# Performance work log

Measured on AMD Instinct MI355X. Metric: run time of the kernel, lower is better.

Reference implementation:

```python
import jax, jax.numpy as jnp
import numpy as np

VOCAB, H, HEADS, S, FF = 100, 8, 2, 6, 16
HD = H // HEADS  # head_dim = 4
EPS = 1e-5


def _layernorm(x, g, b):
    mu = jnp.mean(x, axis=-1, keepdims=True)
    var = jnp.mean((x - mu) ** 2, axis=-1, keepdims=True)
    return (x - mu) * jax.lax.rsqrt(var + EPS) * g + b


def setup_inputs() -> dict:
    key = jax.random.key(0)
    ks = jax.random.split(key, 20)
    B = 262144
    d = {
        'input_ids': jax.random.randint(ks[0], (B, S), 0, VOCAB),
        'tok_emb': jax.random.normal(ks[1], (VOCAB, H), jnp.float32) * 0.02,
        'pos_emb': jax.random.normal(ks[2], (S, H), jnp.float32) * 0.02,
        'Wq': jax.random.normal(ks[3], (H, H), jnp.float32) * 0.1,
        'bq': jnp.zeros((H,), jnp.float32),
        'Wk': jax.random.normal(ks[4], (H, H), jnp.float32) * 0.1,
        'bk': jnp.zeros((H,), jnp.float32),
        'Wv': jax.random.normal(ks[5], (H, H), jnp.float32) * 0.1,
        'bv': jnp.zeros((H,), jnp.float32),
        'Wo': jax.random.normal(ks[6], (H, H), jnp.float32) * 0.1,
        'bo': jnp.zeros((H,), jnp.float32),
        'W1': jax.random.normal(ks[7], (FF, H), jnp.float32) * 0.1,
        'b1': jnp.zeros((FF,), jnp.float32),
        'W2': jax.random.normal(ks[8], (H, FF), jnp.float32) * 0.1,
        'b2': jnp.zeros((H,), jnp.float32),
        'g1': jnp.ones((H,), jnp.float32),
        'be1': jnp.zeros((H,), jnp.float32),
        'g2': jnp.ones((H,), jnp.float32),
        'be2': jnp.zeros((H,), jnp.float32),
    }
    return d


def reference(input_ids, tok_emb, pos_emb, Wq, bq, Wk, bk, Wv, bv, Wo, bo,
              W1, b1, W2, b2, g1, be1, g2, be2):
    B, Sq = input_ids.shape
    x = tok_emb[input_ids] + pos_emb[None, :, :]  # [B,S,H]
    q = x @ Wq.T + bq
    k = x @ Wk.T + bk
    v = x @ Wv.T + bv
    # split heads: [B, heads, S, head_dim]
    q = q.reshape(B, Sq, HEADS, HD).transpose(0, 2, 1, 3)
    k = k.reshape(B, Sq, HEADS, HD).transpose(0, 2, 1, 3)
    v = v.reshape(B, Sq, HEADS, HD).transpose(0, 2, 1, 3)
    scores = jnp.einsum('bhsd,bhtd->bhst', q, k) / (HD ** 0.5)
    probs = jax.nn.softmax(scores, axis=-1)
    attn = jnp.einsum('bhst,bhtd->bhsd', probs, v)
    attn = attn.transpose(0, 2, 1, 3).reshape(B, Sq, H)
    attn = attn @ Wo.T + bo
    h = _layernorm(x + attn, g1, be1)
    ffn = jax.nn.gelu(h @ W1.T + b1, approximate=False) @ W2.T + b2
    return _layernorm(h + ffn, g2, be2)
```

## Files before the change

kernel.cpp:

```cpp
#include <hip/hip_runtime.h>

#define TT_S 6
#define TT_H 8
#define TT_FF 16
#define SEQ_PER_BLK 64
#define BLK 384
#define KV_STRIDE_U 52

typedef __fp16 h2_t __attribute__((ext_vector_type(2)));
typedef __fp16 h8_t __attribute__((ext_vector_type(8)));

__device__ __forceinline__ unsigned pk2(float a, float b) {
  h2_t h = __builtin_amdgcn_cvt_pkrtz(a, b);
  return __builtin_bit_cast(unsigned, h);
}

__global__ __launch_bounds__(BLK, 6) void tt_fused(
    const int* __restrict__ ids,
    const float* __restrict__ tok_emb, const float* __restrict__ pos_emb,
    const float* __restrict__ Wq, const float* __restrict__ bq,
    const float* __restrict__ Wk, const float* __restrict__ bk,
    const float* __restrict__ Wv, const float* __restrict__ bv,
    const float* __restrict__ Wo, const float* __restrict__ bo,
    const float* __restrict__ W1, const float* __restrict__ b1,
    const float* __restrict__ W2, const float* __restrict__ b2,
    const float* __restrict__ g1, const float* __restrict__ be1,
    const float* __restrict__ g2, const float* __restrict__ be2,
    float* __restrict__ out, int B)
{
  __shared__ __align__(16) unsigned s_kv[SEQ_PER_BLK * KV_STRIDE_U];
  __shared__ __align__(16) unsigned s_tok[400];

  const int tid = threadIdx.x;
  for (int i = tid; i < 400; i += BLK) {
    float2 tv = ((const float2*)tok_emb)[i];
    s_tok[i] = pk2(tv.x, tv.y);
  }
  __syncthreads();

  const int s_loc = tid / TT_S;
  const int t     = tid - s_loc * TT_S;
  const int seq_g = blockIdx.x * SEQ_PER_BLK + s_loc;
  const bool valid = (seq_g < B);
  const size_t gidx = (size_t)blockIdx.x * BLK + tid;
  const int id = valid ? ids[gidx] : 0;

  h8_t t0 = ((const h8_t*)s_tok)[id];
  const float4* pr = (const float4*)(pos_emb + t * TT_H);
  float4 p0 = pr[0];
  float4 p1 = pr[1];
  float xs[TT_H];
  xs[0] = (float)t0[0] + p0.x; xs[1] = (float)t0[1] + p0.y;
  xs[2] = (float)t0[2] + p0.z; xs[3] = (float)t0[3] + p0.w;
  xs[4] = (float)t0[4] + p1.x; xs[5] = (float)t0[5] + p1.y;
  xs[6] = (float)t0[6] + p1.z; xs[7] = (float)t0[7] + p1.w;

  {
    float kr[TT_H], vr[TT_H];
    #pragma unroll
    for (int i = 0; i < TT_H; ++i) {
      float ak = bk[i], av = bv[i];
      #pragma unroll
      for (int j = 0; j < TT_H; ++j) {
        ak = fmaf(xs[j], Wk[i*8+j], ak);
        av = fmaf(xs[j], Wv[i*8+j], av);
      }
      kr[i] = ak; vr[i] = av;
    }
    unsigned* kvp = s_kv + s_loc * KV_STRIDE_U + t * 8;
    uint4 w0, w1;
    w0.x = pk2(kr[0], kr[1]); w0.y = pk2(kr[2], kr[3]);
    w0.z = pk2(kr[4], kr[5]); w0.w = pk2(kr[6], kr[7]);
    w1.x = pk2(vr[0], vr[1]); w1.y = pk2(vr[2], vr[3]);
    w1.z = pk2(vr[4], vr[5]); w1.w = pk2(vr[6], vr[7]);
    ((uint4*)kvp)[0] = w0;
    ((uint4*)kvp)[1] = w1;
  }
  __syncthreads();

  float qs[TT_H];
  #pragma unroll
  for (int i = 0; i < TT_H; ++i) {
    float a = bq[i];
    #pragma unroll
    for (int j = 0; j < TT_H; ++j) a = fmaf(xs[j], Wq[i*8+j], a);
    qs[i] = a;
  }

  float acc[TT_H] = {0.f,0.f,0.f,0.f,0.f,0.f,0.f,0.f};
  float sum0 = 0.f, sum1 = 0.f;
  const h8_t* kvb = (const h8_t*)(s_kv + s_loc * KV_STRIDE_U);
  #pragma unroll
  for (int t2 = 0; t2 < TT_S; ++t2) {
    h8_t kh = kvb[t2*2];
    h8_t vh = kvb[t2*2+1];
    float d0 = (float)kh[0] * qs[0];
    d0 = fmaf((float)kh[1], qs[1], d0);
    d0 = fmaf((float)kh[2], qs[2], d0);
    d0 = fmaf((float)kh[3], qs[3], d0);
    float d1 = (float)kh[4] * qs[4];
    d1 = fmaf((float)kh[5], qs[5], d1);
    d1 = fmaf((float)kh[6], qs[6], d1);
    d1 = fmaf((float)kh[7], qs[7], d1);
    float e0 = __builtin_amdgcn_exp2f(d0 * 0.7213475204f);
    float e1 = __builtin_amdgcn_exp2f(d1 * 0.7213475204f);
    sum0 += e0; sum1 += e1;
    acc[0] = fmaf(e0, (float)vh[0], acc[0]);
    acc[1] = fmaf(e0, (float)vh[1], acc[1]);
    acc[2] = fmaf(e0, (float)vh[2], acc[2]);
    acc[3] = fmaf(e0, (float)vh[3], acc[3]);
    acc[4] = fmaf(e1, (float)vh[4], acc[4]);
    acc[5] = fmaf(e1, (float)vh[5], acc[5]);
    acc[6] = fmaf(e1, (float)vh[6], acc[6]);
    acc[7] = fmaf(e1, (float)vh[7], acc[7]);
  }
  {
    float inv0 = __builtin_amdgcn_rcpf(sum0);
    float inv1 = __builtin_amdgcn_rcpf(sum1);
    acc[0] *= inv0; acc[1] *= inv0; acc[2] *= inv0; acc[3] *= inv0;
    acc[4] *= inv1; acc[5] *= inv1; acc[6] *= inv1; acc[7] *= inv1;
  }

  float r[TT_H];
  float mu = 0.f;
  #pragma unroll
  for (int i = 0; i < TT_H; ++i) {
    float o = bo[i];
    #pragma unroll
    for (int j = 0; j < TT_H; ++j) o = fmaf(acc[j], Wo[i*8+j], o);
    r[i] = xs[i] + o;
    mu += r[i];
  }
  mu *= 0.125f;
  float var = 0.f;
  #pragma unroll
  for (int i = 0; i < TT_H; ++i) { float d = r[i] - mu; var = fmaf(d, d, var); }
  float rin = __builtin_amdgcn_rsqf(fmaf(var, 0.125f, 1e-5f));
  float mc = mu * rin;
  float hr[TT_H];
  #pragma unroll
  for (int i = 0; i < TT_H; ++i)
    hr[i] = fmaf(fmaf(r[i], rin, -mc), g1[i], be1[i]);

  float f1[TT_FF];
  #pragma unroll
  for (int f = 0; f < TT_FF; ++f) {
    float u = b1[f];
    #pragma unroll
    for (int j = 0; j < TT_H; ++j) u = fmaf(hr[j], W1[f*8+j], u);
    float u2 = u * u;
    float e  = __builtin_amdgcn_exp2f(u * fmaf(0.1029432f, u2, 2.3022072f));
    float rr = __builtin_amdgcn_rcpf(e + 1.0f);
    f1[f] = fmaf(-u, rr, u);
  }

  float r2[TT_H];
  float mu2 = 0.f;
  #pragma unroll
  for (int i = 0; i < TT_H; ++i) {
    float y = b2[i];
    #pragma unroll
    for (int f = 0; f < TT_FF; ++f) y = fmaf(f1[f], W2[i*16+f], y);
    r2[i] = hr[i] + y;
    mu2 += r2[i];
  }
  mu2 *= 0.125f;
  float var2 = 0.f;
  #pragma unroll
  for (int i = 0; i < TT_H; ++i) { float d = r2[i] - mu2; var2 = fmaf(d, d, var2); }
  float rin2 = __builtin_amdgcn_rsqf(fmaf(var2, 0.125f, 1e-5f));
  float mc2 = mu2 * rin2;

  if (valid) {
    float res[TT_H];
    #pragma unroll
    for (int i = 0; i < TT_H; ++i)
      res[i] = fmaf(fmaf(r2[i], rin2, -mc2), g2[i], be2[i]);
    float* op = out + gidx * TT_H;
    float4 v0; v0.x = res[0]; v0.y = res[1]; v0.z = res[2]; v0.w = res[3];
    float4 v1; v1.x = res[4]; v1.y = res[5]; v1.z = res[6]; v1.w = res[7];
    ((float4*)op)[0] = v0;
    ((float4*)op)[1] = v1;
  }
}

extern "C" void kernel_launch(void* const* d_in, const int* in_sizes, int n_in,
                              void* d_out, int out_size, void* d_ws, size_t ws_size,
                              hipStream_t stream) {
  const int*   ids = (const int*)  d_in[0];
  const float* tok = (const float*)d_in[1];
  const float* pos = (const float*)d_in[2];
  const float* Wq  = (const float*)d_in[3];
  const float* bq  = (const float*)d_in[4];
  const float* Wk  = (const float*)d_in[5];
  const float* bk  = (const float*)d_in[6];
  const float* Wv  = (const float*)d_in[7];
  const float* bv  = (const float*)d_in[8];
  const float* Wo  = (const float*)d_in[9];
  const float* bo  = (const float*)d_in[10];
  const float* W1  = (const float*)d_in[11];
  const float* b1  = (const float*)d_in[12];
  const float* W2  = (const float*)d_in[13];
  const float* b2  = (const float*)d_in[14];
  const float* g1  = (const float*)d_in[15];
  const float* be1 = (const float*)d_in[16];
  const float* g2  = (const float*)d_in[17];
  const float* be2 = (const float*)d_in[18];
  float* out = (float*)d_out;

  const int B = in_sizes[0] / TT_S;
  const int grid = (B + SEQ_PER_BLK - 1) / SEQ_PER_BLK;
  hipLaunchKernelGGL(tt_fused, dim3(grid), dim3(BLK), 0, stream,
                     ids, tok, pos, Wq, bq, Wk, bk, Wv, bv, Wo, bo,
                     W1, b1, W2, b2, g1, be1, g2, be2, out, B);
}
```

Baseline: 142.5 us.

## Use packed fp16 dot2 instructions for all projections via prepacked weights

Adds a small prep kernel that converts all weight matrices and positional embeddings to packed fp16 pairs in the workspace. The main kernel then does the Q/K/V, output, and both FFN projections, plus the attention scores, with v_dot2 fp16 instructions accumulating in fp32. This roughly halves the ALU instruction count and the number of scalar weight loads. In exchange it adds an extra launch and loses accuracy because activations are rounded to fp16 before each matmul.

Result: no change. 144.1 us (+1.1%).

```diff
diff --git a/kernel.cpp b/kernel.cpp
--- a/kernel.cpp
+++ b/kernel.cpp
@@ -7,23 +7,65 @@
 #define BLK 384
 #define KV_STRIDE_U 52
 
-typedef __fp16 h2_t __attribute__((ext_vector_type(2)));
-typedef __fp16 h8_t __attribute__((ext_vector_type(8)));
+#define WQH  0
+#define WKH  32
+#define WVH  64
+#define WOH  96
+#define W1H  128
+#define W2H  192
+#define POSH 256
+
+typedef __fp16   h2_t  __attribute__((ext_vector_type(2)));
+typedef __fp16   h8_t  __attribute__((ext_vector_type(8)));
+typedef _Float16 f16x2 __attribute__((ext_vector_type(2)));
 
 __device__ __forceinline__ unsigned pk2(float a, float b) {
   h2_t h = __builtin_amdgcn_cvt_pkrtz(a, b);
   return __builtin_bit_cast(unsigned, h);
 }
+__device__ __forceinline__ h2_t pk2h(float a, float b) {
+  return __builtin_amdgcn_cvt_pkrtz(a, b);
+}
+__device__ __forceinline__ h2_t bch(unsigned u) {
+  return __builtin_bit_cast(h2_t, u);
+}
+
+#if __has_builtin(__builtin_amdgcn_fdot2)
+__device__ __forceinline__ float dot2f(h2_t a, h2_t b, float c) {
+  return __builtin_amdgcn_fdot2(__builtin_bit_cast(f16x2, a),
+                                __builtin_bit_cast(f16x2, b), c, false);
+}
+#else
+__device__ __forceinline__ float dot2f(h2_t a, h2_t b, float c) {
+  return fmaf((float)a[0], (float)b[0], fmaf((float)a[1], (float)b[1], c));
+}
+#endif
+
+__global__ void tt_prep(const float* __restrict__ Wq, const float* __restrict__ Wk,
+                        const float* __restrict__ Wv, const float* __restrict__ Wo,
+                        const float* __restrict__ W1, const float* __restrict__ W2,
+                        const float* __restrict__ pos, unsigned* __restrict__ ws)
+{
+  const int i = threadIdx.x;
+  if (i < 128) {
+    const float* Wm = (i < 32) ? Wq : (i < 64) ? Wk : (i < 96) ? Wv : Wo;
+    const int p = i & 31;
+    ws[i] = pk2(Wm[2*p], Wm[2*p+1]);
+  }
+  if (i < 64) {
+    ws[W1H + i] = pk2(W1[2*i], W1[2*i+1]);
+    ws[W2H + i] = pk2(W2[2*i], W2[2*i+1]);
+  }
+  if (i < 24) ws[POSH + i] = pk2(pos[2*i], pos[2*i+1]);
+}
 
 __global__ __launch_bounds__(BLK, 6) void tt_fused(
     const int* __restrict__ ids,
-    const float* __restrict__ tok_emb, const float* __restrict__ pos_emb,
-    const float* __restrict__ Wq, const float* __restrict__ bq,
-    const float* __restrict__ Wk, const float* __restrict__ bk,
-    const float* __restrict__ Wv, const float* __restrict__ bv,
-    const float* __restrict__ Wo, const float* __restrict__ bo,
-    const float* __restrict__ W1, const float* __restrict__ b1,
-    const float* __restrict__ W2, const float* __restrict__ b2,
+    const float* __restrict__ tok_emb,
+    const unsigned* __restrict__ wsu,
+    const float* __restrict__ bq, const float* __restrict__ bk,
+    const float* __restrict__ bv, const float* __restrict__ bo,
+    const float* __restrict__ b1, const float* __restrict__ b2,
     const float* __restrict__ g1, const float* __restrict__ be1,
     const float* __restrict__ g2, const float* __restrict__ be2,
     float* __restrict__ out, int B)
@@ -45,26 +87,32 @@
   const size_t gidx = (size_t)blockIdx.x * BLK + tid;
   const int id = valid ? ids[gidx] : 0;
 
-  h8_t t0 = ((const h8_t*)s_tok)[id];
-  const float4* pr = (const float4*)(pos_emb + t * TT_H);
-  float4 p0 = pr[0];
-  float4 p1 = pr[1];
-  float xs[TT_H];
-  xs[0] = (float)t0[0] + p0.x; xs[1] = (float)t0[1] + p0.y;
-  xs[2] = (float)t0[2] + p0.z; xs[3] = (float)t0[3] + p0.w;
-  xs[4] = (float)t0[4] + p1.x; xs[5] = (float)t0[5] + p1.y;
-  xs[6] = (float)t0[6] + p1.z; xs[7] = (float)t0[7] + p1.w;
+  uint4 tw = ((const uint4*)s_tok)[id];
+  uint4 pw = ((const uint4*)(wsu + POSH))[t];
+  h2_t xs0 = bch(tw.x) + bch(pw.x);
+  h2_t xs1 = bch(tw.y) + bch(pw.y);
+  h2_t xs2 = bch(tw.z) + bch(pw.z);
+  h2_t xs3 = bch(tw.w) + bch(pw.w);
+
+  float xf[TT_H];
+  xf[0] = (float)xs0[0]; xf[1] = (float)xs0[1];
+  xf[2] = (float)xs1[0]; xf[3] = (float)xs1[1];
+  xf[4] = (float)xs2[0]; xf[5] = (float)xs2[1];
+  xf[6] = (float)xs3[0]; xf[7] = (float)xs3[1];
 
   {
     float kr[TT_H], vr[TT_H];
     #pragma unroll
     for (int i = 0; i < TT_H; ++i) {
       float ak = bk[i], av = bv[i];
-      #pragma unroll
-      for (int j = 0; j < TT_H; ++j) {
-        ak = fmaf(xs[j], Wk[i*8+j], ak);
-        av = fmaf(xs[j], Wv[i*8+j], av);
-      }
+      ak = dot2f(xs0, bch(wsu[WKH + i*4 + 0]), ak);
+      ak = dot2f(xs1, bch(wsu[WKH + i*4 + 1]), ak);
+      ak = dot2f(xs2, bch(wsu[WKH + i*4 + 2]), ak);
+      ak = dot2f(xs3, bch(wsu[WKH + i*4 + 3]), ak);
+      av = dot2f(xs0, bch(wsu[WVH + i*4 + 0]), av);
+      av = dot2f(xs1, bch(wsu[WVH + i*4 + 1]), av);
+      av = dot2f(xs2, bch(wsu[WVH + i*4 + 2]), av);
+      av = dot2f(xs3, bch(wsu[WVH + i*4 + 3]), av);
       kr[i] = ak; vr[i] = av;
     }
     unsigned* kvp = s_kv + s_loc * KV_STRIDE_U + t * 8;
@@ -78,33 +126,36 @@
   }
   __syncthreads();
 
-  float qs[TT_H];
-  #pragma unroll
-  for (int i = 0; i < TT_H; ++i) {
-    float a = bq[i];
-    #pragma unroll
-    for (int j = 0; j < TT_H; ++j) a = fmaf(xs[j], Wq[i*8+j], a);
-    qs[i] = a;
+  h2_t qh[4];
+  #pragma unroll
+  for (int i = 0; i < 4; ++i) {
+    float a0 = bq[2*i], a1 = bq[2*i+1];
+    a0 = dot2f(xs0, bch(wsu[WQH + (2*i)*4 + 0]), a0);
+    a0 = dot2f(xs1, bch(wsu[WQH + (2*i)*4 + 1]), a0);
+    a0 = dot2f(xs2, bch(wsu[WQH + (2*i)*4 + 2]), a0);
+    a0 = dot2f(xs3, bch(wsu[WQH + (2*i)*4 + 3]), a0);
+    a1 = dot2f(xs0, bch(wsu[WQH + (2*i+1)*4 + 0]), a1);
+    a1 = dot2f(xs1, bch(wsu[WQH + (2*i+1)*4 + 1]), a1);
+    a1 = dot2f(xs2, bch(wsu[WQH + (2*i+1)*4 + 2]), a1);
+    a1 = dot2f(xs3, bch(wsu[WQH + (2*i+1)*4 + 3]), a1);
+    qh[i] = pk2h(a0 * 0.7213475204f, a1 * 0.7213475204f);
   }
 
   float acc[TT_H] = {0.f,0.f,0.f,0.f,0.f,0.f,0.f,0.f};
   float sum0 = 0.f, sum1 = 0.f;
-  const h8_t* kvb = (const h8_t*)(s_kv + s_loc * KV_STRIDE_U);
+  const uint4* kvb = (const uint4*)(s_kv + s_loc * KV_STRIDE_U);
   #pragma unroll
   for (int t2 = 0; t2 < TT_S; ++t2) {
-    h8_t kh = kvb[t2*2];
-    h8_t vh = kvb[t2*2+1];
-    float d0 = (float)kh[0] * qs[0];
-    d0 = fmaf((float)kh[1], qs[1], d0);
-    d0 = fmaf((float)kh[2], qs[2], d0);
-    d0 = fmaf((float)kh[3], qs[3], d0);
-    float d1 = (float)kh[4] * qs[4];
-    d1 = fmaf((float)kh[5], qs[5], d1);
-    d1 = fmaf((float)kh[6], qs[6], d1);
-    d1 = fmaf((float)kh[7], qs[7], d1);
-    float e0 = __builtin_amdgcn_exp2f(d0 * 0.7213475204f);
-    float e1 = __builtin_amdgcn_exp2f(d1 * 0.7213475204f);
+    uint4 kw = kvb[t2*2];
+    uint4 vw = kvb[t2*2+1];
+    float d0 = dot2f(qh[0], bch(kw.x), 0.f);
+    d0 = dot2f(qh[1], bch(kw.y), d0);
+    float d1 = dot2f(qh[2], bch(kw.z), 0.f);
+    d1 = dot2f(qh[3], bch(kw.w), d1);
+    float e0 = __builtin_amdgcn_exp2f(d0);
+    float e1 = __builtin_amdgcn_exp2f(d1);
     sum0 += e0; sum1 += e1;
+    h8_t vh = __builtin_bit_cast(h8_t, vw);
     acc[0] = fmaf(e0, (float)vh[0], acc[0]);
     acc[1] = fmaf(e0, (float)vh[1], acc[1]);
     acc[2] = fmaf(e0, (float)vh[2], acc[2]);
@@ -114,11 +165,14 @@
     acc[6] = fmaf(e1, (float)vh[6], acc[6]);
     acc[7] = fmaf(e1, (float)vh[7], acc[7]);
   }
+  h2_t ah[4];
   {
     float inv0 = __builtin_amdgcn_rcpf(sum0);
     float inv1 = __builtin_amdgcn_rcpf(sum1);
-    acc[0] *= inv0; acc[1] *= inv0; acc[2] *= inv0; acc[3] *= inv0;
-    acc[4] *= inv1; acc[5] *= inv1; acc[6] *= inv1; acc[7] *= inv1;
+    ah[0] = pk2h(acc[0]*inv0, acc[1]*inv0);
+    ah[1] = pk2h(acc[2]*inv0, acc[3]*inv0);
+    ah[2] = pk2h(acc[4]*inv1, acc[5]*inv1);
+    ah[3] = pk2h(acc[6]*inv1, acc[7]*inv1);
   }
 
   float r[TT_H];
@@ -126,9 +180,11 @@
   #pragma unroll
   for (int i = 0; i < TT_H; ++i) {
     float o = bo[i];
-    #pragma unroll
-    for (int j = 0; j < TT_H; ++j) o = fmaf(acc[j], Wo[i*8+j], o);
-    r[i] = xs[i] + o;
+    o = dot2f(ah[0], bch(wsu[WOH + i*4 + 0]), o);
+    o = dot2f(ah[1], bch(wsu[WOH + i*4 + 1]), o);
+    o = dot2f(ah[2], bch(wsu[WOH + i*4 + 2]), o);
+    o = dot2f(ah[3], bch(wsu[WOH + i*4 + 3]), o);
+    r[i] = xf[i] + o;
     mu += r[i];
   }
   mu *= 0.125f;
@@ -141,17 +197,29 @@
   #pragma unroll
   for (int i = 0; i < TT_H; ++i)
     hr[i] = fmaf(fmaf(r[i], rin, -mc), g1[i], be1[i]);
-
-  float f1[TT_FF];
-  #pragma unroll
-  for (int f = 0; f < TT_FF; ++f) {
-    float u = b1[f];
-    #pragma unroll
-    for (int j = 0; j < TT_H; ++j) u = fmaf(hr[j], W1[f*8+j], u);
-    float u2 = u * u;
-    float e  = __builtin_amdgcn_exp2f(u * fmaf(0.1029432f, u2, 2.3022072f));
-    float rr = __builtin_amdgcn_rcpf(e + 1.0f);
-    f1[f] = fmaf(-u, rr, u);
+  h2_t hh[4];
+  hh[0] = pk2h(hr[0], hr[1]);
+  hh[1] = pk2h(hr[2], hr[3]);
+  hh[2] = pk2h(hr[4], hr[5]);
+  hh[3] = pk2h(hr[6], hr[7]);
+
+  h2_t fh[8];
+  #pragma unroll
+  for (int f = 0; f < TT_FF; f += 2) {
+    float u0 = b1[f], u1 = b1[f+1];
+    u0 = dot2f(hh[0], bch(wsu[W1H + f*4 + 0]), u0);
+    u0 = dot2f(hh[1], bch(wsu[W1H + f*4 + 1]), u0);
+    u0 = dot2f(hh[2], bch(wsu[W1H + f*4 + 2]), u0);
+    u0 = dot2f(hh[3], bch(wsu[W1H + f*4 + 3]), u0);
+    u1 = dot2f(hh[0], bch(wsu[W1H + f*4 + 4]), u1);
+    u1 = dot2f(hh[1], bch(wsu[W1H + f*4 + 5]), u1);
+    u1 = dot2f(hh[2], bch(wsu[W1H + f*4 + 6]), u1);
+    u1 = dot2f(hh[3], bch(wsu[W1H + f*4 + 7]), u1);
+    float e0 = __builtin_amdgcn_exp2f(u0 * fmaf(0.1029432f, u0*u0, 2.3022072f));
+    float e1 = __builtin_amdgcn_exp2f(u1 * fmaf(0.1029432f, u1*u1, 2.3022072f));
+    float g0 = fmaf(-u0, __builtin_amdgcn_rcpf(e0 + 1.0f), u0);
+    float g1v = fmaf(-u1, __builtin_amdgcn_rcpf(e1 + 1.0f), u1);
+    fh[f>>1] = pk2h(g0, g1v);
   }
 
   float r2[TT_H];
@@ -159,8 +227,14 @@
   #pragma unroll
   for (int i = 0; i < TT_H; ++i) {
     float y = b2[i];
-    #pragma unroll
-    for (int f = 0; f < TT_FF; ++f) y = fmaf(f1[f], W2[i*16+f], y);
+    y = dot2f(fh[0], bch(wsu[W2H + i*8 + 0]), y);
+    y = dot2f(fh[1], bch(wsu[W2H + i*8 + 1]), y);
+    y = dot2f(fh[2], bch(wsu[W2H + i*8 + 2]), y);
+    y = dot2f(fh[3], bch(wsu[W2H + i*8 + 3]), y);
+    y = dot2f(fh[4], bch(wsu[W2H + i*8 + 4]), y);
+    y = dot2f(fh[5], bch(wsu[W2H + i*8 + 5]), y);
+    y = dot2f(fh[6], bch(wsu[W2H + i*8 + 6]), y);
+    y = dot2f(fh[7], bch(wsu[W2H + i*8 + 7]), y);
     r2[i] = hr[i] + y;
     mu2 += r2[i];
   }
@@ -207,10 +281,14 @@
   const float* g2  = (const float*)d_in[17];
   const float* be2 = (const float*)d_in[18];
   float* out = (float*)d_out;
+  unsigned* ws = (unsigned*)d_ws;
+
+  hipLaunchKernelGGL(tt_prep, dim3(1), dim3(128), 0, stream,
+                     Wq, Wk, Wv, Wo, W1, W2, pos, ws);
 
   const int B = in_sizes[0] / TT_S;
   const int grid = (B + SEQ_PER_BLK - 1) / SEQ_PER_BLK;
   hipLaunchKernelGGL(tt_fused, dim3(grid), dim3(BLK), 0, stream,
-                     ids, tok, pos, Wq, bq, Wk, bk, Wv, bv, Wo, bo,
-                     W1, b1, W2, b2, g1, be1, g2, be2, out, B);
-}
+                     ids, tok, ws, bq, bk, bv, bo, b1, b2,
+                     g1, be1, g2, be2, out, B);
+}
```
